# Kernel tuning notes

Measured on AMD Instinct MI355X. Metric: run time of the kernel, lower is better.

Reference implementation:

```python
import jax, jax.numpy as jnp
import numpy as np

N, L, H, D = 8, 1024, 16, 64
HD = H * D          # hidden_size = 1024
MLP = 4 * HD        # mlp_dim = 4096
EPS = 1e-5


def _layer_norm(x, g, b):
    mu = jnp.mean(x, axis=-1, keepdims=True)
    var = jnp.var(x, axis=-1, keepdims=True)
    return (x - mu) * jax.lax.rsqrt(var + EPS) * g + b


def setup_inputs() -> dict:
    key = jax.random.key(0)
    ks = jax.random.split(key, 8)
    s_in = 1.0 / np.sqrt(HD)
    s_mlp = 1.0 / np.sqrt(MLP)
    return {
        "x": jax.random.normal(ks[0], (N, L, HD), jnp.float32),
        "ln0_g": jnp.ones((HD,), jnp.float32),
        "ln0_b": jnp.zeros((HD,), jnp.float32),
        "wq": jax.random.normal(ks[1], (HD, HD), jnp.float32) * s_in,
        "bq": jnp.zeros((HD,), jnp.float32),
        "wk": jax.random.normal(ks[2], (HD, HD), jnp.float32) * s_in,
        "bk": jnp.zeros((HD,), jnp.float32),
        "wv": jax.random.normal(ks[3], (HD, HD), jnp.float32) * s_in,
        "bv": jnp.zeros((HD,), jnp.float32),
        "wo": jax.random.normal(ks[4], (HD, HD), jnp.float32) * s_in,
        "bo": jnp.zeros((HD,), jnp.float32),
        "ln1_g": jnp.ones((HD,), jnp.float32),
        "ln1_b": jnp.zeros((HD,), jnp.float32),
        "w1": jax.random.normal(ks[5], (HD, MLP), jnp.float32) * s_in,
        "b1": jnp.zeros((MLP,), jnp.float32),
        "w2": jax.random.normal(ks[6], (MLP, HD), jnp.float32) * s_mlp,
        "b2": jnp.zeros((HD,), jnp.float32),
    }


def reference(x, ln0_g, ln0_b, wq, bq, wk, bk, wv, bv, wo, bo,
              ln1_g, ln1_b, w1, b1, w2, b2):
    n, l, hd = x.shape
    # --- pre-LN self-attention ---
    y = _layer_norm(x, ln0_g, ln0_b)
    q = (y @ wq + bq).reshape(n, l, H, D)
    k = (y @ wk + bk).reshape(n, l, H, D)
    v = (y @ wv + bv).reshape(n, l, H, D)
    qkt = jnp.einsum('nqhd,nkhd->nqkh', q, k) / jnp.sqrt(jnp.float32(D))
    attn = jax.nn.softmax(qkt, axis=2)
    y = jnp.einsum('nqkh,nkhd->nqhd', attn, v).reshape(n, l, hd)
    y = y @ wo + bo
    x = x + y  # residual (dropout_rate=0 in eval)
    # --- pre-LN MLP ---
    y = _layer_norm(x, ln1_g, ln1_b)
    y = jax.nn.gelu(y @ w1 + b1)
    y = y @ w2 + b2
    return x + y
```

## Files before the change

### kernel.cpp

```cpp
#include <hip/hip_runtime.h>
#include <math.h>

typedef __attribute__((ext_vector_type(8))) __bf16 bf16x8;
typedef __attribute__((ext_vector_type(4))) float f32x4;

#define NBATCH 8
#define SEQ    1024
#define NHEAD  16
#define DHEAD  64
#define HID    1024
#define MLPD   4096

static __device__ __forceinline__ unsigned short f2bf(float f) {
  unsigned int u = __float_as_uint(f);
  u += 0x7fffu + ((u >> 16) & 1u);
  return (unsigned short)(u >> 16);
}

static __device__ __forceinline__ void gload_lds16(const unsigned short* g,
                                                   unsigned short* l) {
  __builtin_amdgcn_global_load_lds(
      (const __attribute__((address_space(1))) unsigned int*)g,
      (__attribute__((address_space(3))) unsigned int*)l, 16, 0, 0);
}

static __device__ __forceinline__ float gelu_fast(float v) {
  const float z = 0.7978845608028654f * (v + 0.044715f * v * v * v);
  const float e = __expf(-2.0f * fabsf(z));
  float th = (1.0f - e) / (1.0f + e);
  th = copysignf(th, z);
  return 0.5f * v * (1.0f + th);
}

__global__ __launch_bounds__(256) void k_transpose(const float* __restrict__ in,
                                                   unsigned short* __restrict__ out,
                                                   int R, int C) {
  __shared__ float t[32][33];
  const int tx = threadIdx.x & 31, ty = threadIdx.x >> 5;
  const int c0 = blockIdx.x * 32, r0 = blockIdx.y * 32;
#pragma unroll
  for (int j = 0; j < 4; ++j)
    t[ty + j * 8][tx] = in[(size_t)(r0 + ty + j * 8) * C + c0 + tx];
  __syncthreads();
#pragma unroll
  for (int j = 0; j < 4; ++j)
    out[(size_t)(c0 + ty + j * 8) * R + r0 + tx] = f2bf(t[tx][ty + j * 8]);
}

__global__ void k_pack_bias(const float* __restrict__ bq, const float* __restrict__ bk,
                            const float* __restrict__ bv, float* __restrict__ o) {
  int i = blockIdx.x * 256 + threadIdx.x;
  if (i < 3 * HID) {
    float v = (i < HID) ? bq[i] : (i < 2 * HID ? bk[i - HID] : bv[i - 2 * HID]);
    o[i] = v;
  }
}

__global__ __launch_bounds__(256) void k_ln(const float* __restrict__ x,
                                            const float* __restrict__ gw,
                                            const float* __restrict__ bw,
                                            unsigned short* __restrict__ y) {
  __shared__ float red[2][4];
  const int row = blockIdx.x;
  const int tid = threadIdx.x;
  const float4 v = ((const float4*)(x + (size_t)row * HID))[tid];
  float sum = v.x + v.y + v.z + v.w;
  float sq  = v.x * v.x + v.y * v.y + v.z * v.z + v.w * v.w;
#pragma unroll
  for (int off = 32; off >= 1; off >>= 1) {
    sum += __shfl_xor(sum, off);
    sq  += __shfl_xor(sq, off);
  }
  if ((tid & 63) == 0) { red[0][tid >> 6] = sum; red[1][tid >> 6] = sq; }
  __syncthreads();
  sum = red[0][0] + red[0][1] + red[0][2] + red[0][3];
  sq  = red[1][0] + red[1][1] + red[1][2] + red[1][3];
  const float mu  = sum * (1.0f / HID);
  const float var = sq * (1.0f / HID) - mu * mu;
  const float rs  = rsqrtf(var + 1e-5f);
  const float4 g4 = ((const float4*)gw)[tid];
  const float4 b4 = ((const float4*)bw)[tid];
  ushort4 ov;
  ov.x = f2bf((v.x - mu) * rs * g4.x + b4.x);
  ov.y = f2bf((v.y - mu) * rs * g4.y + b4.y);
  ov.z = f2bf((v.z - mu) * rs * g4.z + b4.z);
  ov.w = f2bf((v.w - mu) * rs * g4.w + b4.w);
  ((ushort4*)(y + (size_t)row * HID))[tid] = ov;
}

template <int EPI>
__global__ __launch_bounds__(256) void k_gemm(const unsigned short* __restrict__ A,
                                              const unsigned short* __restrict__ BT,
                                              const float* __restrict__ bias,
                                              const float* __restrict__ res,
                                              void* __restrict__ Cout,
                                              int M, int N, int K) {
  __shared__ unsigned short As[2][128 * 32];
  __shared__ unsigned short Bs[2][128 * 32];
  const int tid  = threadIdx.x;
  const int lane = tid & 63;
  const int w    = tid >> 6;
  const int wr   = w >> 1, wc = w & 1;
  const int l15  = lane & 15, g = lane >> 4;

  const int gx = gridDim.x;
  const int nwg = gx * gridDim.y;
  int lid = blockIdx.y * gx + blockIdx.x;
  lid = (lid & 7) * (nwg >> 3) + (lid >> 3);
  const int m0 = (lid / gx) * 128, n0 = (lid % gx) * 128;

  f32x4 acc[4][4] = {};

  const int lrow = lane >> 2;
  const int lcol = (lane & 3) * 8;
  const unsigned short* Ag = A  + (size_t)(m0 + w * 32 + lrow) * K + lcol;
  const unsigned short* Bg = BT + (size_t)(n0 + w * 32 + lrow) * K + lcol;
  const int dst0 = (w * 32) * 32;
  const int dst1 = (w * 32 + 16) * 32;

#define STAGE_G(buf, kk)                                        \
  do {                                                          \
    gload_lds16(Ag + (kk),                 &As[buf][dst0]);     \
    gload_lds16(Ag + (size_t)16 * K + (kk), &As[buf][dst1]);    \
    gload_lds16(Bg + (kk),                 &Bs[buf][dst0]);     \
    gload_lds16(Bg + (size_t)16 * K + (kk), &Bs[buf][dst1]);    \
  } while (0)

  STAGE_G(0, 0);
  __syncthreads();
  int cur = 0;
  for (int k0 = 0; k0 < K; k0 += 32) {
    if (k0 + 32 < K) STAGE_G(cur ^ 1, k0 + 32);
    bf16x8 af[4], bfr[4];
#pragma unroll
    for (int m = 0; m < 4; ++m)
      af[m] = *(const bf16x8*)(&As[cur][(wr * 64 + m * 16 + l15) * 32 + g * 8]);
#pragma unroll
    for (int n = 0; n < 4; ++n)
      bfr[n] = *(const bf16x8*)(&Bs[cur][(wc * 64 + n * 16 + l15) * 32 + g * 8]);
#pragma unroll
    for (int m = 0; m < 4; ++m)
#pragma unroll
      for (int n = 0; n < 4; ++n)
        acc[m][n] = __builtin_amdgcn_mfma_f32_16x16x32_bf16(af[m], bfr[n], acc[m][n], 0, 0, 0);
    __syncthreads();
    cur ^= 1;
  }
#undef STAGE_G

  if constexpr (EPI == 2) {
#pragma unroll
    for (int m = 0; m < 4; ++m) {
#pragma unroll
      for (int n = 0; n < 4; ++n) {
        const int col = n0 + wc * 64 + n * 16 + l15;
        const float bc = bias[col];
#pragma unroll
        for (int r = 0; r < 4; ++r) {
          const int row = m0 + wr * 64 + m * 16 + g * 4 + r;
          const size_t idx = (size_t)row * N + col;
          ((float*)Cout)[idx] = acc[m][n][r] + bc + res[idx];
        }
      }
    }
  } else {
    unsigned short* ep = (w < 2) ? &As[w][0] : &Bs[w - 2][0];
#pragma unroll
    for (int m = 0; m < 4; ++m) {
#pragma unroll
      for (int n = 0; n < 4; ++n) {
        const float bc = bias[n0 + wc * 64 + n * 16 + l15];
#pragma unroll
        for (int r = 0; r < 4; ++r) {
          float v = acc[m][n][r] + bc;
          if constexpr (EPI == 1) v = gelu_fast(v);
          ep[(m * 16 + g * 4 + r) * 64 + n * 16 + l15] = f2bf(v);
        }
      }
    }
#pragma unroll
    for (int j = 0; j < 8; ++j) {
      const int t = lane + j * 64;
      const int row = t >> 3, colb = (t & 7) * 8;
      const uint4 vv = *(const uint4*)(ep + row * 64 + colb);
      unsigned short* outp = (unsigned short*)Cout +
          (size_t)(m0 + wr * 64 + row) * N + n0 + wc * 64 + colb;
      *(uint4*)outp = vv;
    }
  }
}

__global__ __launch_bounds__(256) void k_vt(const unsigned short* __restrict__ qkv,
                                            unsigned short* __restrict__ vT) {
  __shared__ unsigned short t[64][72];
  const int nh = blockIdx.y;
  const int nb = nh >> 4, h = nh & 15;
  const int l0 = blockIdx.x * 64;
  const int tx = threadIdx.x & 7;
  const int ty = threadIdx.x >> 3;
  const unsigned short* src = qkv + (size_t)(nb * SEQ + l0) * 3072 + 2048 + h * DHEAD;
#pragma unroll
  for (int j = 0; j < 2; ++j)
    *(uint4*)(&t[ty + j * 32][tx * 8]) =
        *(const uint4*)(&src[(size_t)(ty + j * 32) * 3072 + tx * 8]);
  __syncthreads();
  unsigned short* dst = vT + (size_t)nh * DHEAD * SEQ + l0;
#pragma unroll
  for (int j = 0; j < 2; ++j) {
    const int d = ty + j * 32;
    ushort4 a, b;
    a.x = t[tx * 8 + 0][d]; a.y = t[tx * 8 + 1][d];
    a.z = t[tx * 8 + 2][d]; a.w = t[tx * 8 + 3][d];
    b.x = t[tx * 8 + 4][d]; b.y = t[tx * 8 + 5][d];
    b.z = t[tx * 8 + 6][d]; b.w = t[tx * 8 + 7][d];
    *(ushort4*)(&dst[(size_t)d * SEQ + tx * 8])     = a;
    *(ushort4*)(&dst[(size_t)d * SEQ + tx * 8 + 4]) = b;
  }
}

#define SOFTMAX_GROUP(S, gq)                                                       \
  {                                                                                \
    float mx = -INFINITY;                                                          \
    _Pragma("unroll") for (int c = 0; c < 4; ++c)                                  \
      _Pragma("unroll") for (int r = 0; r < 4; ++r)                                \
        mx = fmaxf(mx, S[c][r]);                                                   \
    mx = fmaxf(mx, __shfl_xor(mx, 16));                                            \
    mx = fmaxf(mx, __shfl_xor(mx, 32));                                            \
    const float mnew = fmaxf(m_run[gq], mx);                                       \
    const float sc = __expf(0.125f * (m_run[gq] - mnew));                          \
    m_run[gq] = mnew;                                                              \
    float ts = 0.0f;                                                               \
    _Pragma("unroll") for (int c = 0; c < 4; ++c) {                                \
      const float p0 = __expf(0.125f * (S[c][0] - mnew));                          \
      const float p1 = __expf(0.125f * (S[c][1] - mnew));                          \
      const float p2 = __expf(0.125f * (S[c][2] - mnew));                          \
      const float p3 = __expf(0.125f * (S[c][3] - mnew));                          \
      ts += (p0 + p1) + (p2 + p3);                                                 \
      const unsigned int lo = (unsigned int)f2bf(p0) | ((unsigned int)f2bf(p1) << 16); \
      const unsigned int hi = (unsigned int)f2bf(p2) | ((unsigned int)f2bf(p3) << 16); \
      *(uint2*)(&P_lds[w][((gq) * 16 + l15) * 72 + c * 16 + g * 4]) = make_uint2(lo, hi); \
    }                                                                              \
    ts += __shfl_xor(ts, 16);                                                      \
    ts += __shfl_xor(ts, 32);                                                      \
    s_run[gq] = s_run[gq] * sc + ts;                                               \
    const float scr0 = __shfl(sc, g * 4 + 0), scr1 = __shfl(sc, g * 4 + 1);        \
    const float scr2 = __shfl(sc, g * 4 + 2), scr3 = __shfl(sc, g * 4 + 3);        \
    _Pragma("unroll") for (int dt = 0; dt < 4; ++dt) {                             \
      o[gq][dt][0] *= scr0; o[gq][dt][1] *= scr1;                                  \
      o[gq][dt][2] *= scr2; o[gq][dt][3] *= scr3;                                  \
    }                                                                              \
  }

__global__ __launch_bounds__(256, 4) void k_attn(const unsigned short* __restrict__ qkv,
                                                 const unsigned short* __restrict__ vT,
                                                 unsigned short* __restrict__ outp) {
  __shared__ unsigned short Ks[64 * 64];
  __shared__ unsigned short Vs[64 * 64];
  __shared__ unsigned short P_lds[4][32 * 72];
  const int tid  = threadIdx.x;
  const int lane = tid & 63;
  const int w    = tid >> 6;
  const int l15  = lane & 15, g = lane >> 4;
  const int nh = blockIdx.y;
  const int nb = nh >> 4, h = nh & 15;
  const int q0 = blockIdx.x * 128 + w * 32;
  const size_t RS = 3 * HID;

  const unsigned short* Qp = qkv + (size_t)(nb * SEQ + q0) * RS + h * DHEAD;
  const unsigned short* Kg = qkv + (size_t)(nb * SEQ) * RS + HID + h * DHEAD;
  const unsigned short* Vg = vT + (size_t)nh * DHEAD * SEQ;

  const int L0 = tid * 32, L1 = L0 + 16;
  const int kr0 = L0 >> 7, kc0 = (L0 & 127) ^ ((kr0 & 7) << 4);
  const int kr1 = L1 >> 7, kc1 = (L1 & 127) ^ ((kr1 & 7) << 4);

  bf16x8 aq[2][2];
#pragma unroll
  for (int gq = 0; gq < 2; ++gq)
#pragma unroll
    for (int t = 0; t < 2; ++t)
      aq[gq][t] = *(const bf16x8*)(&Qp[(size_t)(gq * 16 + l15) * RS + t * 32 + g * 8]);

  f32x4 o[2][4] = {};
  float m_run[2] = {-INFINITY, -INFINITY};
  float s_run[2] = {0.0f, 0.0f};

  uint4 rk0, rk1, rv0, rv1;
  rk0 = *(const uint4*)(Kg + (size_t)kr0 * RS + (kc0 >> 1));
  rk1 = *(const uint4*)(Kg + (size_t)kr1 * RS + (kc1 >> 1));
  rv0 = *(const uint4*)(Vg + (size_t)kr0 * SEQ + (kc0 >> 1));
  rv1 = *(const uint4*)(Vg + (size_t)kr1 * SEQ + (kc1 >> 1));
  *(uint4*)(&Ks[tid * 16])     = rk0;
  *(uint4*)(&Ks[tid * 16 + 8]) = rk1;
  *(uint4*)(&Vs[tid * 16])     = rv0;
  *(uint4*)(&Vs[tid * 16 + 8]) = rv1;
  __syncthreads();

  const int sw = (l15 & 7) << 4;

  for (int t16 = 0; t16 < 16; ++t16) {
    if (t16 < 15) {
      const int kb = (t16 + 1) * 64;
      rk0 = *(const uint4*)(Kg + (size_t)(kb + kr0) * RS + (kc0 >> 1));
      rk1 = *(const uint4*)(Kg + (size_t)(kb + kr1) * RS + (kc1 >> 1));
      rv0 = *(const uint4*)(Vg + (size_t)kr0 * SEQ + kb + (kc0 >> 1));
      rv1 = *(const uint4*)(Vg + (size_t)kr1 * SEQ + kb + (kc1 >> 1));
    }

    f32x4 S0[4], S1[4];
#pragma unroll
    for (int c = 0; c < 4; ++c) {
      const int krow = c * 16 + l15;
      const bf16x8 k0 = *(const bf16x8*)(&Ks[krow * 64 + ((( 0 + g * 16) ^ sw) >> 1)]);
      const bf16x8 k1 = *(const bf16x8*)(&Ks[krow * 64 + (((64 + g * 16) ^ sw) >> 1)]);
      f32x4 a = {};
      a = __builtin_amdgcn_mfma_f32_16x16x32_bf16(k0, aq[0][0], a, 0, 0, 0);
      a = __builtin_amdgcn_mfma_f32_16x16x32_bf16(k1, aq[0][1], a, 0, 0, 0);
      S0[c] = a;
      f32x4 b = {};
      b = __builtin_amdgcn_mfma_f32_16x16x32_bf16(k0, aq[1][0], b, 0, 0, 0);
      b = __builtin_amdgcn_mfma_f32_16x16x32_bf16(k1, aq[1][1], b, 0, 0, 0);
      S1[c] = b;
    }

    SOFTMAX_GROUP(S0, 0)
    SOFTMAX_GROUP(S1, 1)

    bf16x8 pa[2][2];
#pragma unroll
    for (int gq = 0; gq < 2; ++gq)
#pragma unroll
      for (int th = 0; th < 2; ++th)
        pa[gq][th] = *(const bf16x8*)(&P_lds[w][(gq * 16 + l15) * 72 + th * 32 + g * 8]);
#pragma unroll
    for (int dt = 0; dt < 4; ++dt) {
      const int vrow = dt * 16 + l15;
      const bf16x8 v0 = *(const bf16x8*)(&Vs[vrow * 64 + ((( 0 + g * 16) ^ sw) >> 1)]);
      const bf16x8 v1 = *(const bf16x8*)(&Vs[vrow * 64 + (((64 + g * 16) ^ sw) >> 1)]);
      o[0][dt] = __builtin_amdgcn_mfma_f32_16x16x32_bf16(pa[0][0], v0, o[0][dt], 0, 0, 0);
      o[0][dt] = __builtin_amdgcn_mfma_f32_16x16x32_bf16(pa[0][1], v1, o[0][dt], 0, 0, 0);
      o[1][dt] = __builtin_amdgcn_mfma_f32_16x16x32_bf16(pa[1][0], v0, o[1][dt], 0, 0, 0);
      o[1][dt] = __builtin_amdgcn_mfma_f32_16x16x32_bf16(pa[1][1], v1, o[1][dt], 0, 0, 0);
    }
    __syncthreads();
    if (t16 < 15) {
      *(uint4*)(&Ks[tid * 16])     = rk0;
      *(uint4*)(&Ks[tid * 16 + 8]) = rk1;
      *(uint4*)(&Vs[tid * 16])     = rv0;
      *(uint4*)(&Vs[tid * 16 + 8]) = rv1;
      __syncthreads();
    }
  }

#pragma unroll
  for (int gq = 0; gq < 2; ++gq) {
    float sr[4];
#pragma unroll
    for (int r = 0; r < 4; ++r) sr[r] = 1.0f / __shfl(s_run[gq], g * 4 + r);
#pragma unroll
    for (int dt = 0; dt < 4; ++dt)
#pragma unroll
      for (int r = 0; r < 4; ++r)
        outp[(size_t)(nb * SEQ + q0 + gq * 16 + g * 4 + r) * HID + h * DHEAD + dt * 16 + l15] =
            f2bf(o[gq][dt][r] * sr[r]);
  }
}

extern "C" void kernel_launch(void* const* d_in, const int* in_sizes, int n_in,
                              void* d_out, int out_size, void* d_ws, size_t ws_size,
                              hipStream_t stream) {
  const float* x    = (const float*)d_in[0];
  const float* ln0g = (const float*)d_in[1];
  const float* ln0b = (const float*)d_in[2];
  const float* wq   = (const float*)d_in[3];
  const float* bq   = (const float*)d_in[4];
  const float* wk   = (const float*)d_in[5];
  const float* bk   = (const float*)d_in[6];
  const float* wv   = (const float*)d_in[7];
  const float* bv   = (const float*)d_in[8];
  const float* wo   = (const float*)d_in[9];
  const float* bo   = (const float*)d_in[10];
  const float* ln1g = (const float*)d_in[11];
  const float* ln1b = (const float*)d_in[12];
  const float* w1   = (const float*)d_in[13];
  const float* b1   = (const float*)d_in[14];
  const float* w2   = (const float*)d_in[15];
  const float* b2   = (const float*)d_in[16];
  float* out = (float*)d_out;

  char* ws = (char*)d_ws;
  unsigned short* qkvT = (unsigned short*)(ws + 0);
  unsigned short* woT  = (unsigned short*)(ws + 6291456);
  unsigned short* w1T  = (unsigned short*)(ws + 8388608);
  unsigned short* w2T  = (unsigned short*)(ws + 16777216);
  float*          bqkv = (float*)(ws + 25165824);
  unsigned short* ybuf = (unsigned short*)(ws + 25178112);
  unsigned short* qkv  = (unsigned short*)(ws + 41955328);
  unsigned short* att  = (unsigned short*)(ws + 92286976);
  unsigned short* hbuf = qkv;
  unsigned short* vT   = ybuf;

  const int M = NBATCH * SEQ;

  k_transpose<<<dim3(32, 32),  256, 0, stream>>>(wq, qkvT,                        HID,  HID);
  k_transpose<<<dim3(32, 32),  256, 0, stream>>>(wk, qkvT + (size_t)1024 * HID,   HID,  HID);
  k_transpose<<<dim3(32, 32),  256, 0, stream>>>(wv, qkvT + (size_t)2048 * HID,   HID,  HID);
  k_transpose<<<dim3(32, 32),  256, 0, stream>>>(wo, woT,                         HID,  HID);
  k_transpose<<<dim3(128, 32), 256, 0, stream>>>(w1, w1T,                         HID,  MLPD);
  k_transpose<<<dim3(32, 128), 256, 0, stream>>>(w2, w2T,                         MLPD, HID);
  k_pack_bias<<<dim3(12), 256, 0, stream>>>(bq, bk, bv, bqkv);

  k_ln<<<dim3(M), 256, 0, stream>>>(x, ln0g, ln0b, ybuf);
  k_gemm<0><<<dim3(24, 64), 256, 0, stream>>>(ybuf, qkvT, bqkv, nullptr, (void*)qkv, M, 3 * HID, HID);
  k_vt<<<dim3(16, 128), 256, 0, stream>>>(qkv, vT);
  k_attn<<<dim3(8, 128), 256, 0, stream>>>(qkv, vT, att);
  k_gemm<2><<<dim3(8, 64), 256, 0, stream>>>(att, woT, bo, x, (void*)out, M, HID, HID);
  k_ln<<<dim3(M), 256, 0, stream>>>(out, ln1g, ln1b, ybuf);
  k_gemm<1><<<dim3(32, 64), 256, 0, stream>>>(ybuf, w1T, b1, nullptr, (void*)hbuf, M, MLPD, HID);
  k_gemm<2><<<dim3(8, 64), 256, 0, stream>>>(hbuf, w2T, b2, out, (void*)out, M, HID, MLPD);
}
```

Before: 441.5 us.

## Rewrite GEMM with 256-row tiles, 8 waves, swizzled LDS and K=64 stages

Replaces the 128x128, 4-wave GEMM with 256xBN tiles (BN=128 or 256) run by 512-thread blocks. Each k-step now covers 64 elements, and the LDS layout is XOR-swizzled to avoid bank conflicts. Explicit barriers, waitcnt and setprio interleave the MFMA groups across waves. This is meant to raise data reuse per tile and MFMA throughput, at the cost of more LDS and registers per block, fewer blocks in some launches, and dropping the grouped block-order remap.

```diff
diff --git a/kernel.cpp b/kernel.cpp
--- a/kernel.cpp
+++ b/kernel.cpp
@@ -88,103 +88,136 @@
   ((ushort4*)(y + (size_t)row * HID))[tid] = ov;
 }
 
-template <int EPI>
-__global__ __launch_bounds__(256) void k_gemm(const unsigned short* __restrict__ A,
-                                              const unsigned short* __restrict__ BT,
-                                              const float* __restrict__ bias,
-                                              const float* __restrict__ res,
-                                              void* __restrict__ Cout,
-                                              int M, int N, int K) {
-  __shared__ unsigned short As[2][128 * 32];
-  __shared__ unsigned short Bs[2][128 * 32];
+template <int EPI, int BN>
+__global__ __launch_bounds__(512, 2) void k_gemm(const unsigned short* __restrict__ A,
+                                                 const unsigned short* __restrict__ BT,
+                                                 const float* __restrict__ bias,
+                                                 const float* __restrict__ res,
+                                                 void* __restrict__ Cout,
+                                                 int M, int N, int K) {
+  constexpr int ASZ = 256 * 64;
+  constexpr int BSZ = BN * 64;
+  constexpr int NF  = BN / 64;
+  constexpr int NCW = BN / 4;
+  constexpr int BCALLS = BN / 64;
+  __shared__ unsigned short sh[2 * ASZ + 2 * BSZ];
+
   const int tid  = threadIdx.x;
   const int lane = tid & 63;
   const int w    = tid >> 6;
-  const int wr   = w >> 1, wc = w & 1;
+  const int wr   = w >> 2, wc = w & 3;
   const int l15  = lane & 15, g = lane >> 4;
-
-  const int gx = gridDim.x;
-  const int nwg = gx * gridDim.y;
-  int lid = blockIdx.y * gx + blockIdx.x;
-  lid = (lid & 7) * (nwg >> 3) + (lid >> 3);
-  const int m0 = (lid / gx) * 128, n0 = (lid % gx) * 128;
-
-  f32x4 acc[4][4] = {};
-
-  const int lrow = lane >> 2;
-  const int lcol = (lane & 3) * 8;
-  const unsigned short* Ag = A  + (size_t)(m0 + w * 32 + lrow) * K + lcol;
-  const unsigned short* Bg = BT + (size_t)(n0 + w * 32 + lrow) * K + lcol;
-  const int dst0 = (w * 32) * 32;
-  const int dst1 = (w * 32 + 16) * 32;
-
-#define STAGE_G(buf, kk)                                        \
-  do {                                                          \
-    gload_lds16(Ag + (kk),                 &As[buf][dst0]);     \
-    gload_lds16(Ag + (size_t)16 * K + (kk), &As[buf][dst1]);    \
-    gload_lds16(Bg + (kk),                 &Bs[buf][dst0]);     \
-    gload_lds16(Bg + (size_t)16 * K + (kk), &Bs[buf][dst1]);    \
+  const int m0 = blockIdx.y * 256, n0 = blockIdx.x * BN;
+
+  f32x4 acc[8][NF] = {};
+
+  const int srow  = w * 8 + (lane >> 3);
+  const int scolb = ((lane & 7) * 16) ^ (((lane >> 3) & 7) << 4);
+  const unsigned short* pA = A  + (size_t)(m0 + srow) * K + (scolb >> 1);
+  const unsigned short* pB = BT + (size_t)(n0 + srow) * K + (scolb >> 1);
+  unsigned short* shB = sh + 2 * ASZ;
+
+#define STAGE(buf, kk)                                                          \
+  do {                                                                          \
+    _Pragma("unroll") for (int c = 0; c < 4; ++c)                               \
+      gload_lds16(pA + (size_t)c * 64 * K + (kk),                               \
+                  sh + (buf) * ASZ + (c * 64 + w * 8) * 64);                    \
+    _Pragma("unroll") for (int c = 0; c < BCALLS; ++c)                          \
+      gload_lds16(pB + (size_t)c * 64 * K + (kk),                               \
+                  shB + (buf) * BSZ + (c * 64 + w * 8) * 64);                   \
   } while (0)
 
-  STAGE_G(0, 0);
-  __syncthreads();
-  int cur = 0;
-  for (int k0 = 0; k0 < K; k0 += 32) {
-    if (k0 + 32 < K) STAGE_G(cur ^ 1, k0 + 32);
-    bf16x8 af[4], bfr[4];
-#pragma unroll
-    for (int m = 0; m < 4; ++m)
-      af[m] = *(const bf16x8*)(&As[cur][(wr * 64 + m * 16 + l15) * 32 + g * 8]);
-#pragma unroll
-    for (int n = 0; n < 4; ++n)
-      bfr[n] = *(const bf16x8*)(&Bs[cur][(wc * 64 + n * 16 + l15) * 32 + g * 8]);
-#pragma unroll
-    for (int m = 0; m < 4; ++m)
-#pragma unroll
-      for (int n = 0; n < 4; ++n)
-        acc[m][n] = __builtin_amdgcn_mfma_f32_16x16x32_bf16(af[m], bfr[n], acc[m][n], 0, 0, 0);
-    __syncthreads();
-    cur ^= 1;
-  }
-#undef STAGE_G
+  const int fmask = (l15 & 7) << 4;
+  const int bo0 = ((0 * 64) + g * 16) ^ fmask;
+  const int bo1 = ((1 * 64) + g * 16) ^ fmask;
+  const int aRowBase = wr * 128 + l15;
+  const int bRowBase = wc * NCW + l15;
+
+  const int NT = K >> 6;
+
+  STAGE(0, 0);
+  int buf = 0;
+  for (int t = 0; t < NT; ++t) {
+    asm volatile("s_waitcnt vmcnt(0)" ::: "memory");
+    __builtin_amdgcn_sched_barrier(0);
+    __builtin_amdgcn_s_barrier();
+    if (t + 1 < NT) STAGE(buf ^ 1, (t + 1) * 64);
+
+    const unsigned short* shAb = sh + buf * ASZ;
+    const unsigned short* shBb = shB + buf * BSZ;
+
+    bf16x8 bfr[NF][2];
+#pragma unroll
+    for (int n = 0; n < NF; ++n) {
+      const int br = (bRowBase + n * 16) * 64;
+      bfr[n][0] = *(const bf16x8*)(shBb + br + (bo0 >> 1));
+      bfr[n][1] = *(const bf16x8*)(shBb + br + (bo1 >> 1));
+    }
+
+#pragma unroll
+    for (int p = 0; p < 4; ++p) {
+      const int ar0 = (aRowBase + (2 * p) * 16) * 64;
+      const int ar1 = (aRowBase + (2 * p + 1) * 16) * 64;
+      const bf16x8 a00 = *(const bf16x8*)(shAb + ar0 + (bo0 >> 1));
+      const bf16x8 a01 = *(const bf16x8*)(shAb + ar0 + (bo1 >> 1));
+      const bf16x8 a10 = *(const bf16x8*)(shAb + ar1 + (bo0 >> 1));
+      const bf16x8 a11 = *(const bf16x8*)(shAb + ar1 + (bo1 >> 1));
+      __builtin_amdgcn_s_barrier();
+      asm volatile("s_waitcnt lgkmcnt(0)" ::: "memory");
+      __builtin_amdgcn_sched_barrier(0);
+      __builtin_amdgcn_s_setprio(1);
+#pragma unroll
+      for (int n = 0; n < NF; ++n) {
+        acc[2 * p][n]     = __builtin_amdgcn_mfma_f32_16x16x32_bf16(a00, bfr[n][0], acc[2 * p][n], 0, 0, 0);
+        acc[2 * p][n]     = __builtin_amdgcn_mfma_f32_16x16x32_bf16(a01, bfr[n][1], acc[2 * p][n], 0, 0, 0);
+        acc[2 * p + 1][n] = __builtin_amdgcn_mfma_f32_16x16x32_bf16(a10, bfr[n][0], acc[2 * p + 1][n], 0, 0, 0);
+        acc[2 * p + 1][n] = __builtin_amdgcn_mfma_f32_16x16x32_bf16(a11, bfr[n][1], acc[2 * p + 1][n], 0, 0, 0);
+      }
+      __builtin_amdgcn_s_setprio(0);
+      __builtin_amdgcn_s_barrier();
+    }
+    buf ^= 1;
+  }
+#undef STAGE
 
   if constexpr (EPI == 2) {
 #pragma unroll
-    for (int m = 0; m < 4; ++m) {
-#pragma unroll
-      for (int n = 0; n < 4; ++n) {
-        const int col = n0 + wc * 64 + n * 16 + l15;
+    for (int m = 0; m < 8; ++m) {
+#pragma unroll
+      for (int n = 0; n < NF; ++n) {
+        const int col = n0 + wc * NCW + n * 16 + l15;
         const float bc = bias[col];
 #pragma unroll
         for (int r = 0; r < 4; ++r) {
-          const int row = m0 + wr * 64 + m * 16 + g * 4 + r;
+          const int row = m0 + wr * 128 + m * 16 + g * 4 + r;
           const size_t idx = (size_t)row * N + col;
           ((float*)Cout)[idx] = acc[m][n][r] + bc + res[idx];
         }
       }
     }
   } else {
-    unsigned short* ep = (w < 2) ? &As[w][0] : &Bs[w - 2][0];
-#pragma unroll
-    for (int m = 0; m < 4; ++m) {
-#pragma unroll
-      for (int n = 0; n < 4; ++n) {
-        const float bc = bias[n0 + wc * 64 + n * 16 + l15];
+    unsigned short* ep = sh + w * (128 * NCW);
+#pragma unroll
+    for (int m = 0; m < 8; ++m) {
+#pragma unroll
+      for (int n = 0; n < NF; ++n) {
+        const float bc = bias[n0 + wc * NCW + n * 16 + l15];
 #pragma unroll
         for (int r = 0; r < 4; ++r) {
           float v = acc[m][n][r] + bc;
           if constexpr (EPI == 1) v = gelu_fast(v);
-          ep[(m * 16 + g * 4 + r) * 64 + n * 16 + l15] = f2bf(v);
+          ep[(m * 16 + g * 4 + r) * NCW + n * 16 + l15] = f2bf(v);
         }
       }
     }
-#pragma unroll
-    for (int j = 0; j < 8; ++j) {
+    constexpr int CPR = NCW / 8;
+#pragma unroll
+    for (int j = 0; j < NCW / 4; ++j) {
       const int t = lane + j * 64;
-      const int row = t >> 3, colb = (t & 7) * 8;
-      const uint4 vv = *(const uint4*)(ep + row * 64 + colb);
+      const int row = t / CPR, colb = (t % CPR) * 8;
+      const uint4 vv = *(const uint4*)(ep + row * NCW + colb);
       unsigned short* outp = (unsigned short*)Cout +
-          (size_t)(m0 + wr * 64 + row) * N + n0 + wc * 64 + colb;
+          (size_t)(m0 + wr * 128 + row) * N + n0 + wc * NCW + colb;
       *(uint4*)outp = vv;
     }
   }
@@ -411,11 +444,11 @@
   k_pack_bias<<<dim3(12), 256, 0, stream>>>(bq, bk, bv, bqkv);
 
   k_ln<<<dim3(M), 256, 0, stream>>>(x, ln0g, ln0b, ybuf);
-  k_gemm<0><<<dim3(24, 64), 256, 0, stream>>>(ybuf, qkvT, bqkv, nullptr, (void*)qkv, M, 3 * HID, HID);
+  k_gemm<0, 128><<<dim3(24, 32), 512, 0, stream>>>(ybuf, qkvT, bqkv, nullptr, (void*)qkv, M, 3 * HID, HID);
   k_vt<<<dim3(16, 128), 256, 0, stream>>>(qkv, vT);
   k_attn<<<dim3(8, 128), 256, 0, stream>>>(qkv, vT, att);
-  k_gemm<2><<<dim3(8, 64), 256, 0, stream>>>(att, woT, bo, x, (void*)out, M, HID, HID);
+  k_gemm<2, 128><<<dim3(8, 32), 512, 0, stream>>>(att, woT, bo, x, (void*)out, M, HID, HID);
   k_ln<<<dim3(M), 256, 0, stream>>>(out, ln1g, ln1b, ybuf);
-  k_gemm<1><<<dim3(32, 64), 256, 0, stream>>>(ybuf, w1T, b1, nullptr, (void*)hbuf, M, MLPD, HID);
-  k_gemm<2><<<dim3(8, 64), 256, 0, stream>>>(hbuf, w2T, b2, out, (void*)out, M, HID, MLPD);
-}
+  k_gemm<1, 256><<<dim3(16, 32), 512, 0, stream>>>(ybuf, w1T, b1, nullptr, (void*)hbuf, M, MLPD, HID);
+  k_gemm<2, 128><<<dim3(8, 32), 512, 0, stream>>>(hbuf, w2T, b2, out, (void*)out, M, HID, MLPD);
+}
```

Measured after the change: 399.3 us. -9.6%, faster.
